# Kernel tuning notes

Measured on AMD Instinct MI355X. Metric: run time of the kernel, lower is better.

The kernel has to match this reference:

```python
import jax, jax.numpy as jnp
import numpy as np

PI = 3.141592653589793
N, B, DIM, HEADS = 4, 8192, 1024, 4
HD = DIM // HEADS  # head_dim = 256


def setup_inputs() -> dict:
    key = jax.random.key(0)
    ks = jax.random.split(key, 10)
    glorot = jax.nn.initializers.glorot_uniform()
    return {
        "axis_embeddings": jax.random.normal(ks[0], (N, B, DIM), jnp.float32),
        "arg_embeddings": jax.random.uniform(ks[1], (N, B, DIM), jnp.float32),
        "W_axis1": glorot(ks[2], (HD, 2 * HD), jnp.float32),
        "b_axis1": jnp.zeros((HD,), jnp.float32),
        "W_arg1": glorot(ks[3], (HD, 2 * HD), jnp.float32),
        "b_arg1": jnp.zeros((HD,), jnp.float32),
        "W_axis2": glorot(ks[4], (HD, HD), jnp.float32),
        "b_axis2": jnp.zeros((HD,), jnp.float32),
        "W_arg2": glorot(ks[5], (HD, HD), jnp.float32),
        "b_arg2": jnp.zeros((HD,), jnp.float32),
    }


def _linear(x, W, b):
    return jnp.einsum('...i,oi->...o', x, W) + b


def reference(axis_embeddings, arg_embeddings, W_axis1, b_axis1, W_arg1, b_arg1,
              W_axis2, b_axis2, W_arg2, b_arg2):
    axis = axis_embeddings.reshape(N, B, HEADS, HD)
    arg = arg_embeddings.reshape(N, B, HEADS, HD)
    al = axis - arg / 2
    ah = axis + arg / 2
    logits = jnp.concatenate([al, ah], axis=-1)  # [N,B,H,2*HD]

    # axis branch: attention over N then circular mean via atan2-style correction
    axis_h1 = jax.nn.relu(_linear(logits, W_axis1, b_axis1))
    axis_attn = jax.nn.softmax(_linear(axis_h1, W_axis2, b_axis2), axis=0)
    x_emb = jnp.sum(axis_attn * jnp.cos(axis), axis=0)  # [B,H,HD]
    y_emb = jnp.sum(axis_attn * jnp.sin(axis), axis=0)
    x_emb = jnp.where(jnp.abs(x_emb) < 0.001, 0.001, x_emb)
    axis_out = jnp.arctan(y_emb / x_emb)
    ind_x = x_emb < 0
    ind_y = y_emb < 0
    ind_two = ind_x & jnp.logical_not(ind_y)
    ind_three = ind_x & ind_y
    axis_out = axis_out + PI * ind_two.astype(axis_out.dtype) - PI * ind_three.astype(axis_out.dtype)

    # arg branch: mean-pooled gate, min over N (dropout p=0 -> identity)
    arg_h1 = jax.nn.relu(_linear(logits, W_arg1, b_arg1))
    gate = jax.nn.sigmoid(_linear(jnp.mean(arg_h1, axis=0), W_arg2, b_arg2))
    arg_out = jnp.min(arg, axis=0) * gate

    return axis_out.reshape(B, DIM), arg_out.reshape(B, DIM)
```

## Files before the change

kernel.cpp:

```cpp
#include <hip/hip_runtime.h>


typedef __attribute__((ext_vector_type(8))) _Float16 f16x8;
typedef __attribute__((ext_vector_type(8))) float f32x8;
typedef __attribute__((ext_vector_type(4))) float f32x4;

#define BH 32768
#define OUT_ARG_OFF 8388608

#define O_WXA_H 0
#define O_WXA_L 65536
#define O_WXR_H 131072
#define O_WXR_L 196608
#define O_WRA_H 262144
#define O_WRR_H 327680
#define O_W2X_H 393216
#define O_W2X_L 458752
#define O_W2G_H 524288
#define WS_HALFS 589824

__device__ __forceinline__ void split16(float x, _Float16& hi, _Float16& lo) {
  float xs = x * 16.0f;
  _Float16 h = (_Float16)xs;
  hi = h;
  lo = (_Float16)(xs - (float)h);
}

__device__ __forceinline__ int fragidx(int o, int k) {
  int ct = o >> 4, kk = k >> 5, lg = (k >> 3) & 3, l15 = o & 15, j = k & 7;
  return (ct * 8 + kk) * 512 + (lg * 16 + l15) * 8 + j;
}

__global__ void combine_weights(const float* __restrict__ Wx1, const float* __restrict__ Wr1,
                                const float* __restrict__ W2x, const float* __restrict__ W2g,
                                _Float16* __restrict__ ws) {
  int i = blockIdx.x * 256 + threadIdx.x;
  int o = i >> 8, k = i & 255;
  int d = fragidx(o, k);
  float a = Wx1[o * 512 + k], b = Wx1[o * 512 + 256 + k];
  _Float16 h, l;
  split16(a + b, h, l);          ws[O_WXA_H + d] = h; ws[O_WXA_L + d] = l;
  split16(0.5f * (b - a), h, l); ws[O_WXR_H + d] = h; ws[O_WXR_L + d] = l;
  a = Wr1[o * 512 + k]; b = Wr1[o * 512 + 256 + k];
  ws[O_WRA_H + d] = (_Float16)((a + b) * 16.0f);
  ws[O_WRR_H + d] = (_Float16)((0.5f * (b - a)) * 16.0f);
  split16(W2x[o * 256 + k], h, l); ws[O_W2X_H + d] = h; ws[O_W2X_L + d] = l;
  ws[O_W2G_H + d] = (_Float16)(W2g[o * 256 + k] * 16.0f);
}

#define MFMA16 __builtin_amdgcn_mfma_f32_16x16x32_f16

__device__ __forceinline__ void stage64(const float* __restrict__ src, int g0, int tid,
                                        _Float16* bufH, _Float16* bufL) {
  #pragma unroll
  for (int c = 0; c < 4; ++c) {
    const int i   = c * 512 + tid;
    const int row = i >> 5;
    const int col = (i & 31) * 8;
    const int gofs = ((row & 3) * BH + g0 + (row >> 2)) * 256 + col;
    f32x8 v = *(const f32x8*)(src + gofs);
    f16x8 xh, xl;
    #pragma unroll
    for (int j = 0; j < 8; ++j) { _Float16 h, lo2; split16(v[j], h, lo2); xh[j] = h; xl[j] = lo2; }
    const int ad = row * 256 + (col ^ ((row & 7) << 3));
    *(f16x8*)(bufH + ad) = xh;
    *(f16x8*)(bufL + ad) = xl;
  }
}

__device__ __forceinline__ void gemm1_pass(const _Float16* __restrict__ ws,
                                           int oBh, int oBl, int oBm,
                                           const _Float16* bufH, const _Float16* bufL,
                                           int ct0, int l, int l15, int lg,
                                           f32x4 (&acc1)[4][2], f32x4 (&accm)[4][2]) {
  f16x8 wh[3][2], wl[3][2], wm[3][2];
  #pragma unroll
  for (int p = 0; p < 2; ++p)
    #pragma unroll
    for (int nt = 0; nt < 2; ++nt) {
      const int fb = (((ct0 + nt) << 3) + p) * 512 + l * 8;
      wh[p][nt] = *(const f16x8*)(ws + oBh + fb);
      wl[p][nt] = *(const f16x8*)(ws + oBl + fb);
      wm[p][nt] = *(const f16x8*)(ws + oBm + fb);
    }
  #pragma unroll
  for (int kk = 0; kk < 8; ++kk) {
    const int cs = kk % 3, ns = (kk + 2) % 3;
    if (kk < 6) {
      #pragma unroll
      for (int nt = 0; nt < 2; ++nt) {
        const int fb = (((ct0 + nt) << 3) + (kk + 2)) * 512 + l * 8;
        wh[ns][nt] = *(const f16x8*)(ws + oBh + fb);
        wl[ns][nt] = *(const f16x8*)(ws + oBl + fb);
        wm[ns][nt] = *(const f16x8*)(ws + oBm + fb);
      }
    }
    f16x8 ah[4], al[4];
    #pragma unroll
    for (int mt = 0; mt < 4; ++mt) {
      const int row = (mt << 4) + l15;
      const int ad  = row * 256 + (((kk << 5) + (lg << 3)) ^ ((row & 7) << 3));
      ah[mt] = *(const f16x8*)(bufH + ad);
      al[mt] = *(const f16x8*)(bufL + ad);
    }
    #pragma unroll
    for (int nt = 0; nt < 2; ++nt)
      #pragma unroll
      for (int mt = 0; mt < 4; ++mt) {
        acc1[mt][nt] = MFMA16(ah[mt], wh[cs][nt], acc1[mt][nt], 0, 0, 0);
        acc1[mt][nt] = MFMA16(al[mt], wh[cs][nt], acc1[mt][nt], 0, 0, 0);
        acc1[mt][nt] = MFMA16(ah[mt], wl[cs][nt], acc1[mt][nt], 0, 0, 0);
        accm[mt][nt] = MFMA16(ah[mt], wm[cs][nt], accm[mt][nt], 0, 0, 0);
      }
  }
}

__global__ __launch_bounds__(512, 2)
void cone_main(const float* __restrict__ axisF, const float* __restrict__ argF,
               const float* __restrict__ bx1, const float* __restrict__ br1,
               const float* __restrict__ bg2,
               const _Float16* __restrict__ ws, float* __restrict__ out)
{
  __shared__ __align__(16) _Float16 lds[36864];
  _Float16* bufH = lds;
  _Float16* bufL = lds + 16384;
  _Float16* h1m  = lds + 32768;

  const int tid = threadIdx.x;
  const int w   = tid >> 6;
  const int l   = tid & 63;
  const int l15 = l & 15;
  const int lg  = l >> 4;
  int bid = blockIdx.x;
  bid = ((bid & 7) << 8) + (bid >> 3);
  const int g0 = bid << 4;
  const float s = 1.0f / 256.0f;
  const int ct0 = w << 1;

  f32x4 acc1[4][2], accm[4][2];
  #pragma unroll
  for (int mt = 0; mt < 4; ++mt)
    #pragma unroll
    for (int nt = 0; nt < 2; ++nt) { acc1[mt][nt] = (f32x4){0,0,0,0}; accm[mt][nt] = (f32x4){0,0,0,0}; }

  stage64(axisF, g0, tid, bufH, bufL);
  __syncthreads();
  gemm1_pass(ws, O_WXA_H, O_WXA_L, O_WRA_H, bufH, bufL, ct0, l, l15, lg, acc1, accm);
  __syncthreads();

  stage64(argF, g0, tid, bufH, bufL);
  __syncthreads();
  gemm1_pass(ws, O_WXR_H, O_WXR_L, O_WRR_H, bufH, bufL, ct0, l, l15, lg, acc1, accm);
  __syncthreads();

  #pragma unroll
  for (int nt = 0; nt < 2; ++nt) {
    const int c  = (w << 5) + (nt << 4) + l15;
    const float bvx = bx1[c];
    const float bvr = br1[c];
    #pragma unroll
    for (int mt = 0; mt < 4; ++mt) {
      #pragma unroll
      for (int r = 0; r < 4; ++r) {
        const int row = (mt << 4) + (lg << 2) + r;
        const float v = fmaxf(acc1[mt][nt][r] * s + bvx, 0.f);
        _Float16 h, lo2; split16(v, h, lo2);
        const int ad = row * 256 + (c ^ ((row & 7) << 3));
        bufH[ad] = h; bufL[ad] = lo2;
      }
      const int p = (mt << 2) + lg;
      float sm = 0.f;
      #pragma unroll
      for (int r = 0; r < 4; ++r) sm += fmaxf(accm[mt][nt][r] * s + bvr, 0.f);
      h1m[p * 256 + (c ^ ((p & 7) << 3))] = (_Float16)(0.25f * sm * 16.0f);
    }
  }
  __syncthreads();

  _Float16* h1h = bufH;
  _Float16* h1l = bufL;
  f32x4 acc2[4][2];
  f32x4 acc3[2];
  #pragma unroll
  for (int mt = 0; mt < 4; ++mt) { acc2[mt][0] = (f32x4){0,0,0,0}; acc2[mt][1] = (f32x4){0,0,0,0}; }
  acc3[0] = (f32x4){0,0,0,0}; acc3[1] = (f32x4){0,0,0,0};
  {
    f16x8 wh[3][2], wl[3][2], wg[3][2];
    f16x8 a2h[2][4], a2l[2][4], am[2];
    #pragma unroll
    for (int p = 0; p < 2; ++p)
      #pragma unroll
      for (int nt = 0; nt < 2; ++nt) {
        const int fb = (((ct0 + nt) << 3) + p) * 512 + l * 8;
        wh[p][nt] = *(const f16x8*)(ws + O_W2X_H + fb);
        wl[p][nt] = *(const f16x8*)(ws + O_W2X_L + fb);
        wg[p][nt] = *(const f16x8*)(ws + O_W2G_H + fb);
      }
    #pragma unroll
    for (int mt = 0; mt < 4; ++mt) {
      const int row = (mt << 4) + l15;
      const int ad  = row * 256 + ((lg << 3) ^ ((row & 7) << 3));
      a2h[0][mt] = *(const f16x8*)(h1h + ad);
      a2l[0][mt] = *(const f16x8*)(h1l + ad);
    }
    am[0] = *(const f16x8*)(h1m + l15 * 256 + ((lg << 3) ^ ((l15 & 7) << 3)));
    #pragma unroll
    for (int kk = 0; kk < 8; ++kk) {
      const int cs = kk % 3, ns = (kk + 2) % 3, ab = kk & 1, an = ab ^ 1;
      if (kk < 6) {
        #pragma unroll
        for (int nt = 0; nt < 2; ++nt) {
          const int fb = (((ct0 + nt) << 3) + (kk + 2)) * 512 + l * 8;
          wh[ns][nt] = *(const f16x8*)(ws + O_W2X_H + fb);
          wl[ns][nt] = *(const f16x8*)(ws + O_W2X_L + fb);
          wg[ns][nt] = *(const f16x8*)(ws + O_W2G_H + fb);
        }
      }
      if (kk < 7) {
        #pragma unroll
        for (int mt = 0; mt < 4; ++mt) {
          const int row = (mt << 4) + l15;
          const int ad  = row * 256 + ((((kk + 1) << 5) + (lg << 3)) ^ ((row & 7) << 3));
          a2h[an][mt] = *(const f16x8*)(h1h + ad);
          a2l[an][mt] = *(const f16x8*)(h1l + ad);
        }
        am[an] = *(const f16x8*)(h1m + l15 * 256 + ((((kk + 1) << 5) + (lg << 3)) ^ ((l15 & 7) << 3)));
      }
      #pragma unroll
      for (int nt = 0; nt < 2; ++nt) {
        #pragma unroll
        for (int mt = 0; mt < 4; ++mt) {
          acc2[mt][nt] = MFMA16(a2h[ab][mt], wh[cs][nt], acc2[mt][nt], 0, 0, 0);
          acc2[mt][nt] = MFMA16(a2l[ab][mt], wh[cs][nt], acc2[mt][nt], 0, 0, 0);
          acc2[mt][nt] = MFMA16(a2h[ab][mt], wl[cs][nt], acc2[mt][nt], 0, 0, 0);
        }
        acc3[nt] = MFMA16(am[ab], wg[cs][nt], acc3[nt], 0, 0, 0);
      }
    }
  }

  #pragma unroll
  for (int nt = 0; nt < 2; ++nt) {
    const int c = (w << 5) + (nt << 4) + l15;
    #pragma unroll
    for (int mt = 0; mt < 4; ++mt) {
      float lv[4];
      #pragma unroll
      for (int r = 0; r < 4; ++r) lv[r] = acc2[mt][nt][r] * s;
      const float mx = fmaxf(fmaxf(lv[0], lv[1]), fmaxf(lv[2], lv[3]));
      float e[4]; float sum = 0.f;
      #pragma unroll
      for (int r = 0; r < 4; ++r) { e[r] = __expf(lv[r] - mx); sum += e[r]; }
      const float inv = 1.f / sum;
      const int g = g0 + (mt << 2) + lg;
      float x = 0.f, y = 0.f;
      #pragma unroll
      for (int r = 0; r < 4; ++r) {
        const float av = axisF[(r * BH + g) * 256 + c];
        float sn, cs2;
        __sincosf(av, &sn, &cs2);
        const float at = e[r] * inv;
        x += at * cs2;
        y += at * sn;
      }
      if (fabsf(x) < 0.001f) x = 0.001f;
      out[g * 256 + c] = atan2f(y, x);
    }
  }

  #pragma unroll
  for (int nt = 0; nt < 2; ++nt) {
    const int c = (w << 5) + (nt << 4) + l15;
    const float bgv = bg2[c];
    #pragma unroll
    for (int r = 0; r < 4; ++r) {
      const int p = (lg << 2) + r;
      const int g = g0 + p;
      const float gate = 1.f / (1.f + __expf(-(acc3[nt][r] * s + bgv)));
      float mn = argF[g * 256 + c];
      #pragma unroll
      for (int n = 1; n < 4; ++n)
        mn = fminf(mn, argF[(n * BH + g) * 256 + c]);
      out[OUT_ARG_OFF + g * 256 + c] = mn * gate;
    }
  }
}

extern "C" void kernel_launch(void* const* d_in, const int* in_sizes, int n_in,
                              void* d_out, int out_size, void* d_ws, size_t ws_size,
                              hipStream_t stream) {
  const float* axisF = (const float*)d_in[0];
  const float* argF  = (const float*)d_in[1];
  const float* Wx1   = (const float*)d_in[2];
  const float* bx1   = (const float*)d_in[3];
  const float* Wr1   = (const float*)d_in[4];
  const float* br1   = (const float*)d_in[5];
  const float* W2x   = (const float*)d_in[6];
  const float* W2g   = (const float*)d_in[8];
  const float* bg2   = (const float*)d_in[9];
  float* out = (float*)d_out;
  _Float16* ws = (_Float16*)d_ws;

  combine_weights<<<256, 256, 0, stream>>>(Wx1, Wr1, W2x, W2g, ws);
  cone_main<<<2048, 512, 0, stream>>>(axisF, argF, bx1, br1, bg2, ws, out);
}
```

Before: 306.9 us.

## Double block M-tile to 32 groups so each weight fragment is reused across 128 rows

Each workgroup now processes 32 batch-head groups (128 rows) instead of 16, halving the grid and doubling the staged LDS tiles and accumulator arrays. Weight fragments loaded from global memory are amortised over twice as many MFMA tiles, which cuts weight traffic per output. The weight prefetch drops from triple to double buffering, and A-operand loads are no longer prefetched. The cost is higher register and LDS use (about 144KB of LDS), which likely limits residency to one block per CU and risks spills under the 512x2 launch bounds.

```diff
diff --git a/kernel.cpp b/kernel.cpp
--- a/kernel.cpp
+++ b/kernel.cpp
@@ -50,10 +50,10 @@
 
 #define MFMA16 __builtin_amdgcn_mfma_f32_16x16x32_f16
 
-__device__ __forceinline__ void stage64(const float* __restrict__ src, int g0, int tid,
-                                        _Float16* bufH, _Float16* bufL) {
-  #pragma unroll
-  for (int c = 0; c < 4; ++c) {
+__device__ __forceinline__ void stage128(const float* __restrict__ src, int g0, int tid,
+                                         _Float16* bufH, _Float16* bufL) {
+  #pragma unroll
+  for (int c = 0; c < 8; ++c) {
     const int i   = c * 512 + tid;
     const int row = i >> 5;
     const int col = (i & 31) * 8;
@@ -68,50 +68,52 @@
   }
 }
 
-__device__ __forceinline__ void gemm1_pass(const _Float16* __restrict__ ws,
-                                           int oBh, int oBl, int oBm,
-                                           const _Float16* bufH, const _Float16* bufL,
-                                           int ct0, int l, int l15, int lg,
-                                           f32x4 (&acc1)[4][2], f32x4 (&accm)[4][2]) {
-  f16x8 wh[3][2], wl[3][2], wm[3][2];
-  #pragma unroll
-  for (int p = 0; p < 2; ++p)
-    #pragma unroll
-    for (int nt = 0; nt < 2; ++nt) {
-      const int fb = (((ct0 + nt) << 3) + p) * 512 + l * 8;
-      wh[p][nt] = *(const f16x8*)(ws + oBh + fb);
-      wl[p][nt] = *(const f16x8*)(ws + oBl + fb);
-      wm[p][nt] = *(const f16x8*)(ws + oBm + fb);
-    }
+__device__ __forceinline__ void gemm1_pass128(const _Float16* __restrict__ ws,
+                                              int oBh, int oBl, int oBm,
+                                              const _Float16* bufH, const _Float16* bufL,
+                                              int ct0, int l, int l15, int lg,
+                                              f32x4 (&acc1)[8][2], f32x4 (&accm)[8][2]) {
+  f16x8 wh[2][2], wl[2][2], wm[2][2];
+  #pragma unroll
+  for (int nt = 0; nt < 2; ++nt) {
+    const int fb = ((ct0 + nt) << 3) * 512 + l * 8;
+    wh[0][nt] = *(const f16x8*)(ws + oBh + fb);
+    wl[0][nt] = *(const f16x8*)(ws + oBl + fb);
+    wm[0][nt] = *(const f16x8*)(ws + oBm + fb);
+  }
   #pragma unroll
   for (int kk = 0; kk < 8; ++kk) {
-    const int cs = kk % 3, ns = (kk + 2) % 3;
-    if (kk < 6) {
+    const int cur = kk & 1, nx = cur ^ 1;
+    if (kk < 7) {
       #pragma unroll
       for (int nt = 0; nt < 2; ++nt) {
-        const int fb = (((ct0 + nt) << 3) + (kk + 2)) * 512 + l * 8;
-        wh[ns][nt] = *(const f16x8*)(ws + oBh + fb);
-        wl[ns][nt] = *(const f16x8*)(ws + oBl + fb);
-        wm[ns][nt] = *(const f16x8*)(ws + oBm + fb);
-      }
-    }
-    f16x8 ah[4], al[4];
-    #pragma unroll
-    for (int mt = 0; mt < 4; ++mt) {
-      const int row = (mt << 4) + l15;
-      const int ad  = row * 256 + (((kk << 5) + (lg << 3)) ^ ((row & 7) << 3));
-      ah[mt] = *(const f16x8*)(bufH + ad);
-      al[mt] = *(const f16x8*)(bufL + ad);
-    }
-    #pragma unroll
-    for (int nt = 0; nt < 2; ++nt)
-      #pragma unroll
-      for (int mt = 0; mt < 4; ++mt) {
-        acc1[mt][nt] = MFMA16(ah[mt], wh[cs][nt], acc1[mt][nt], 0, 0, 0);
-        acc1[mt][nt] = MFMA16(al[mt], wh[cs][nt], acc1[mt][nt], 0, 0, 0);
-        acc1[mt][nt] = MFMA16(ah[mt], wl[cs][nt], acc1[mt][nt], 0, 0, 0);
-        accm[mt][nt] = MFMA16(ah[mt], wm[cs][nt], accm[mt][nt], 0, 0, 0);
-      }
+        const int fb = (((ct0 + nt) << 3) + kk + 1) * 512 + l * 8;
+        wh[nx][nt] = *(const f16x8*)(ws + oBh + fb);
+        wl[nx][nt] = *(const f16x8*)(ws + oBl + fb);
+        wm[nx][nt] = *(const f16x8*)(ws + oBm + fb);
+      }
+    }
+    #pragma unroll
+    for (int grp = 0; grp < 2; ++grp) {
+      f16x8 ah[4], al[4];
+      #pragma unroll
+      for (int q = 0; q < 4; ++q) {
+        const int row = ((grp * 4 + q) << 4) + l15;
+        const int ad  = row * 256 + (((kk << 5) + (lg << 3)) ^ ((row & 7) << 3));
+        ah[q] = *(const f16x8*)(bufH + ad);
+        al[q] = *(const f16x8*)(bufL + ad);
+      }
+      #pragma unroll
+      for (int nt = 0; nt < 2; ++nt)
+        #pragma unroll
+        for (int q = 0; q < 4; ++q) {
+          const int mt = grp * 4 + q;
+          acc1[mt][nt] = MFMA16(ah[q], wh[cur][nt], acc1[mt][nt], 0, 0, 0);
+          acc1[mt][nt] = MFMA16(al[q], wh[cur][nt], acc1[mt][nt], 0, 0, 0);
+          acc1[mt][nt] = MFMA16(ah[q], wl[cur][nt], acc1[mt][nt], 0, 0, 0);
+          accm[mt][nt] = MFMA16(ah[q], wm[cur][nt], accm[mt][nt], 0, 0, 0);
+        }
+    }
   }
 }
 
@@ -121,10 +123,10 @@
                const float* __restrict__ bg2,
                const _Float16* __restrict__ ws, float* __restrict__ out)
 {
-  __shared__ __align__(16) _Float16 lds[36864];
+  __shared__ __align__(16) _Float16 lds[73728];
   _Float16* bufH = lds;
-  _Float16* bufL = lds + 16384;
-  _Float16* h1m  = lds + 32768;
+  _Float16* bufL = lds + 32768;
+  _Float16* h1m  = lds + 65536;
 
   const int tid = threadIdx.x;
   const int w   = tid >> 6;
@@ -132,25 +134,25 @@
   const int l15 = l & 15;
   const int lg  = l >> 4;
   int bid = blockIdx.x;
-  bid = ((bid & 7) << 8) + (bid >> 3);
-  const int g0 = bid << 4;
+  bid = ((bid & 7) << 7) + (bid >> 3);
+  const int g0 = bid << 5;
   const float s = 1.0f / 256.0f;
   const int ct0 = w << 1;
 
-  f32x4 acc1[4][2], accm[4][2];
-  #pragma unroll
-  for (int mt = 0; mt < 4; ++mt)
+  f32x4 acc1[8][2], accm[8][2];
+  #pragma unroll
+  for (int mt = 0; mt < 8; ++mt)
     #pragma unroll
     for (int nt = 0; nt < 2; ++nt) { acc1[mt][nt] = (f32x4){0,0,0,0}; accm[mt][nt] = (f32x4){0,0,0,0}; }
 
-  stage64(axisF, g0, tid, bufH, bufL);
-  __syncthreads();
-  gemm1_pass(ws, O_WXA_H, O_WXA_L, O_WRA_H, bufH, bufL, ct0, l, l15, lg, acc1, accm);
-  __syncthreads();
-
-  stage64(argF, g0, tid, bufH, bufL);
-  __syncthreads();
-  gemm1_pass(ws, O_WXR_H, O_WXR_L, O_WRR_H, bufH, bufL, ct0, l, l15, lg, acc1, accm);
+  stage128(axisF, g0, tid, bufH, bufL);
+  __syncthreads();
+  gemm1_pass128(ws, O_WXA_H, O_WXA_L, O_WRA_H, bufH, bufL, ct0, l, l15, lg, acc1, accm);
+  __syncthreads();
+
+  stage128(argF, g0, tid, bufH, bufL);
+  __syncthreads();
+  gemm1_pass128(ws, O_WXR_H, O_WXR_L, O_WRR_H, bufH, bufL, ct0, l, l15, lg, acc1, accm);
   __syncthreads();
 
   #pragma unroll
@@ -159,7 +161,7 @@
     const float bvx = bx1[c];
     const float bvr = br1[c];
     #pragma unroll
-    for (int mt = 0; mt < 4; ++mt) {
+    for (int mt = 0; mt < 8; ++mt) {
       #pragma unroll
       for (int r = 0; r < 4; ++r) {
         const int row = (mt << 4) + (lg << 2) + r;
@@ -179,62 +181,61 @@
 
   _Float16* h1h = bufH;
   _Float16* h1l = bufL;
-  f32x4 acc2[4][2];
-  f32x4 acc3[2];
-  #pragma unroll
-  for (int mt = 0; mt < 4; ++mt) { acc2[mt][0] = (f32x4){0,0,0,0}; acc2[mt][1] = (f32x4){0,0,0,0}; }
-  acc3[0] = (f32x4){0,0,0,0}; acc3[1] = (f32x4){0,0,0,0};
+  f32x4 acc2[8][2];
+  f32x4 acc3[2][2];
+  #pragma unroll
+  for (int mt = 0; mt < 8; ++mt) { acc2[mt][0] = (f32x4){0,0,0,0}; acc2[mt][1] = (f32x4){0,0,0,0}; }
+  acc3[0][0] = (f32x4){0,0,0,0}; acc3[0][1] = (f32x4){0,0,0,0};
+  acc3[1][0] = (f32x4){0,0,0,0}; acc3[1][1] = (f32x4){0,0,0,0};
   {
-    f16x8 wh[3][2], wl[3][2], wg[3][2];
-    f16x8 a2h[2][4], a2l[2][4], am[2];
-    #pragma unroll
-    for (int p = 0; p < 2; ++p)
-      #pragma unroll
-      for (int nt = 0; nt < 2; ++nt) {
-        const int fb = (((ct0 + nt) << 3) + p) * 512 + l * 8;
-        wh[p][nt] = *(const f16x8*)(ws + O_W2X_H + fb);
-        wl[p][nt] = *(const f16x8*)(ws + O_W2X_L + fb);
-        wg[p][nt] = *(const f16x8*)(ws + O_W2G_H + fb);
-      }
-    #pragma unroll
-    for (int mt = 0; mt < 4; ++mt) {
-      const int row = (mt << 4) + l15;
-      const int ad  = row * 256 + ((lg << 3) ^ ((row & 7) << 3));
-      a2h[0][mt] = *(const f16x8*)(h1h + ad);
-      a2l[0][mt] = *(const f16x8*)(h1l + ad);
-    }
-    am[0] = *(const f16x8*)(h1m + l15 * 256 + ((lg << 3) ^ ((l15 & 7) << 3)));
+    f16x8 wh[2][2], wl[2][2], wg[2][2];
+    #pragma unroll
+    for (int nt = 0; nt < 2; ++nt) {
+      const int fb = ((ct0 + nt) << 3) * 512 + l * 8;
+      wh[0][nt] = *(const f16x8*)(ws + O_W2X_H + fb);
+      wl[0][nt] = *(const f16x8*)(ws + O_W2X_L + fb);
+      wg[0][nt] = *(const f16x8*)(ws + O_W2G_H + fb);
+    }
     #pragma unroll
     for (int kk = 0; kk < 8; ++kk) {
-      const int cs = kk % 3, ns = (kk + 2) % 3, ab = kk & 1, an = ab ^ 1;
-      if (kk < 6) {
+      const int cur = kk & 1, nx = cur ^ 1;
+      if (kk < 7) {
         #pragma unroll
         for (int nt = 0; nt < 2; ++nt) {
-          const int fb = (((ct0 + nt) << 3) + (kk + 2)) * 512 + l * 8;
-          wh[ns][nt] = *(const f16x8*)(ws + O_W2X_H + fb);
-          wl[ns][nt] = *(const f16x8*)(ws + O_W2X_L + fb);
-          wg[ns][nt] = *(const f16x8*)(ws + O_W2G_H + fb);
+          const int fb = (((ct0 + nt) << 3) + kk + 1) * 512 + l * 8;
+          wh[nx][nt] = *(const f16x8*)(ws + O_W2X_H + fb);
+          wl[nx][nt] = *(const f16x8*)(ws + O_W2X_L + fb);
+          wg[nx][nt] = *(const f16x8*)(ws + O_W2G_H + fb);
         }
       }
-      if (kk < 7) {
-        #pragma unroll
-        for (int mt = 0; mt < 4; ++mt) {
-          const int row = (mt << 4) + l15;
-          const int ad  = row * 256 + ((((kk + 1) << 5) + (lg << 3)) ^ ((row & 7) << 3));
-          a2h[an][mt] = *(const f16x8*)(h1h + ad);
-          a2l[an][mt] = *(const f16x8*)(h1l + ad);
+      const int k0 = (kk << 5) + (lg << 3);
+      #pragma unroll
+      for (int grp = 0; grp < 2; ++grp) {
+        f16x8 ah[4], al[4];
+        #pragma unroll
+        for (int q = 0; q < 4; ++q) {
+          const int row = ((grp * 4 + q) << 4) + l15;
+          const int ad  = row * 256 + (k0 ^ ((row & 7) << 3));
+          ah[q] = *(const f16x8*)(h1h + ad);
+          al[q] = *(const f16x8*)(h1l + ad);
         }
-        am[an] = *(const f16x8*)(h1m + l15 * 256 + ((((kk + 1) << 5) + (lg << 3)) ^ ((l15 & 7) << 3)));
-      }
-      #pragma unroll
-      for (int nt = 0; nt < 2; ++nt) {
-        #pragma unroll
-        for (int mt = 0; mt < 4; ++mt) {
-          acc2[mt][nt] = MFMA16(a2h[ab][mt], wh[cs][nt], acc2[mt][nt], 0, 0, 0);
-          acc2[mt][nt] = MFMA16(a2l[ab][mt], wh[cs][nt], acc2[mt][nt], 0, 0, 0);
-          acc2[mt][nt] = MFMA16(a2h[ab][mt], wl[cs][nt], acc2[mt][nt], 0, 0, 0);
-        }
-        acc3[nt] = MFMA16(am[ab], wg[cs][nt], acc3[nt], 0, 0, 0);
+        #pragma unroll
+        for (int nt = 0; nt < 2; ++nt)
+          #pragma unroll
+          for (int q = 0; q < 4; ++q) {
+            const int mt = grp * 4 + q;
+            acc2[mt][nt] = MFMA16(ah[q], wh[cur][nt], acc2[mt][nt], 0, 0, 0);
+            acc2[mt][nt] = MFMA16(al[q], wh[cur][nt], acc2[mt][nt], 0, 0, 0);
+            acc2[mt][nt] = MFMA16(ah[q], wl[cur][nt], acc2[mt][nt], 0, 0, 0);
+          }
+      }
+      #pragma unroll
+      for (int mt2 = 0; mt2 < 2; ++mt2) {
+        const int row2 = (mt2 << 4) + l15;
+        const f16x8 am = *(const f16x8*)(h1m + row2 * 256 + (k0 ^ ((row2 & 7) << 3)));
+        #pragma unroll
+        for (int nt = 0; nt < 2; ++nt)
+          acc3[mt2][nt] = MFMA16(am, wg[cur][nt], acc3[mt2][nt], 0, 0, 0);
       }
     }
   }
@@ -243,7 +244,7 @@
   for (int nt = 0; nt < 2; ++nt) {
     const int c = (w << 5) + (nt << 4) + l15;
     #pragma unroll
-    for (int mt = 0; mt < 4; ++mt) {
+    for (int mt = 0; mt < 8; ++mt) {
       float lv[4];
       #pragma unroll
       for (int r = 0; r < 4; ++r) lv[r] = acc2[mt][nt][r] * s;
@@ -273,15 +274,18 @@
     const int c = (w << 5) + (nt << 4) + l15;
     const float bgv = bg2[c];
     #pragma unroll
-    for (int r = 0; r < 4; ++r) {
-      const int p = (lg << 2) + r;
-      const int g = g0 + p;
-      const float gate = 1.f / (1.f + __expf(-(acc3[nt][r] * s + bgv)));
-      float mn = argF[g * 256 + c];
-      #pragma unroll
-      for (int n = 1; n < 4; ++n)
-        mn = fminf(mn, argF[(n * BH + g) * 256 + c]);
-      out[OUT_ARG_OFF + g * 256 + c] = mn * gate;
+    for (int mt2 = 0; mt2 < 2; ++mt2) {
+      #pragma unroll
+      for (int r = 0; r < 4; ++r) {
+        const int p = (mt2 << 4) + (lg << 2) + r;
+        const int g = g0 + p;
+        const float gate = 1.f / (1.f + __expf(-(acc3[mt2][nt][r] * s + bgv)));
+        float mn = argF[g * 256 + c];
+        #pragma unroll
+        for (int n = 1; n < 4; ++n)
+          mn = fminf(mn, argF[(n * BH + g) * 256 + c]);
+        out[OUT_ARG_OFF + g * 256 + c] = mn * gate;
+      }
     }
   }
 }
@@ -302,5 +306,5 @@
   _Float16* ws = (_Float16*)d_ws;
 
   combine_weights<<<256, 256, 0, stream>>>(Wx1, Wr1, W2x, W2g, ws);
-  cone_main<<<2048, 512, 0, stream>>>(axisF, argF, bx1, br1, bg2, ws, out);
-}
+  cone_main<<<1024, 512, 0, stream>>>(axisF, argF, bx1, br1, bg2, ws, out);
+}
```

After: 487.9 us. 59.0% more time.
